# Performance work log

Hardware: AMD Instinct MI355X
Metric: run time of the kernel (lower is better)

## Reference

```python
import jax, jax.numpy as jnp
import numpy as np


def _div_tree_level(n_agents, level):
    # Deterministic reproduction of get_division_tree (seeded shuffle), row `level`.
    rng = np.random.RandomState(0)
    perm = rng.permutation(n_agents)
    max_div = int(np.ceil(np.log2(n_agents)))
    levels = np.zeros((max_div + 1, n_agents), dtype=np.int64)
    for ith in range(1, max_div + 1):
        levels[ith] = levels[ith - 1]
        for j in range(n_agents):
            seg = j // (n_agents / 2 ** ith)
            if int(seg) % 2 == 1:
                levels[ith, j] += 2 ** (ith - 1)
    res = levels[:, perm]  # res_levels[:, i] = levels[:, agent2divitreeindex[i]]
    return res[level]


def setup_inputs() -> dict:
    B, A, D, H, NA = 4096, 32, 512, 512, 32
    LEVEL = 3  # current_level after change_div_tree_level(3): 8 distinct experts
    key = jax.random.key(0)
    ks = jax.random.split(key, 4)
    x0 = jax.random.normal(ks[0], (B, A, D), dtype=jnp.float32)
    W_shared = jax.random.normal(ks[1], (D, H), dtype=jnp.float32) * 0.02
    b_shared = jnp.zeros((H,), jnp.float32)
    W1 = jax.random.normal(ks[2], (A, H, H), dtype=jnp.float32) * 0.02
    b1 = jnp.zeros((A, H), jnp.float32)
    W2 = jax.random.normal(ks[3], (A, H, NA), dtype=jnp.float32) * 0.02
    b2 = jnp.zeros((A, NA), jnp.float32)
    route = jnp.asarray(_div_tree_level(A, LEVEL), dtype=jnp.int32)  # [A] expert id per agent
    return dict(x0=x0, W_shared=W_shared, b_shared=b_shared,
                W1=W1, b1=b1, W2=W2, b2=b2, route=route)


def reference(x0, W_shared, b_shared, W1, b1, W2, b2, route):
    # shared trunk: Linear + ReLU over all agents at once
    x1 = jax.nn.relu(x0 @ W_shared + b_shared)          # [B, A, H]
    # static MoE dispatch: gather each agent's expert weights, batched GEMM per agent slot
    Wg1, bg1 = W1[route], b1[route]                     # [A, H, H], [A, H]
    Wg2, bg2 = W2[route], b2[route]                     # [A, H, NA], [A, NA]
    h = jax.nn.relu(jnp.einsum('bah,ahk->bak', x1, Wg1) + bg1)   # [B, A, H]
    x2 = jnp.einsum('bah,ahk->bak', h, Wg2) + bg2       # [B, A, NA]
    return x2
```

## Files before the change

kernel.cpp:

```cpp
#include <hip/hip_runtime.h>
#include <cstdint>
#include <cstddef>

typedef __bf16 bf16x8 __attribute__((ext_vector_type(8)));
typedef float f32x4 __attribute__((ext_vector_type(4)));
typedef unsigned short u16;
typedef u16 u16x4 __attribute__((ext_vector_type(4)));

__device__ __forceinline__ u16 f2bf(float f) {
  union { float f; unsigned u; } v; v.f = f;
  return (u16)((v.u + 0x7FFFu + ((v.u >> 16) & 1u)) >> 16);
}

__device__ __forceinline__ void gl_lds16(const void* g, void* l) {
  __builtin_amdgcn_global_load_lds((__attribute__((address_space(1))) void*)(g),
                                   (__attribute__((address_space(3))) void*)(l), 16, 0, 0);
}

__global__ void transpose_cvt(const float* __restrict__ in, const int* __restrict__ route,
                              u16* __restrict__ out, int K, int N) {
  __shared__ float t[32][33];
  const int a = blockIdx.z;
  const int src = route ? route[a] : a;
  const float* ip = in + (size_t)src * K * N;
  u16* op = out + (size_t)a * K * N;
  const int k0 = blockIdx.x * 32, n0 = blockIdx.y * 32;
  const int tx = threadIdx.x, ty = threadIdx.y;
#pragma unroll
  for (int i = 0; i < 4; ++i)
    t[ty + i * 8][tx] = ip[(size_t)(k0 + ty + i * 8) * N + n0 + tx];
  __syncthreads();
#pragma unroll
  for (int i = 0; i < 4; ++i)
    op[(size_t)(n0 + ty + i * 8) * K + k0 + tx] = f2bf(t[tx][ty + i * 8]);
}

__global__ __launch_bounds__(512)
void fused_mlp(const float* __restrict__ X0, const u16* __restrict__ Wst,
               const float* __restrict__ bsh, const u16* __restrict__ W1t,
               const float* __restrict__ b1, const u16* __restrict__ W2t,
               const float* __restrict__ b2, const int* __restrict__ route,
               float* __restrict__ Out) {
  __shared__ u16 lds[69632];
  u16* Xs = lds;
  u16* Bp0 = lds + 32768;
  u16* Bp1 = lds + 49152;
  u16* Ap0 = lds + 65536;
  u16* Ap1 = lds + 67584;

  const int tid = threadIdx.x;
  const int w = tid >> 6, l = tid & 63;
  const int r = l & 15, q = l >> 4;
  const int a = blockIdx.y;
  const int b0 = blockIdx.x * 64;
  const int rt = route[a];

  int aoff[4], boff[4];
#pragma unroll
  for (int t = 0; t < 4; ++t) {
    aoff[t] = (t * 16 + r) * 32 + ((q ^ ((r >> 1) & 3)) << 3);
    boff[t] = (w * 64 + t * 16 + r) * 32 + ((q ^ ((r >> 1) & 3)) << 3);
  }

  int bdst[4]; int bsrc[4];
#pragma unroll
  for (int c = 0; c < 4; ++c) {
    const int p2 = c * 512 + tid;
    const int n = p2 >> 2, s = p2 & 3;
    bsrc[c] = n * 512 + ((s ^ ((n >> 1) & 3)) << 3);
    bdst[c] = p2 * 8;
  }

  const int arow = tid >> 3, akq = tid & 7;
  const float* gA = X0 + ((size_t)(b0 + arow) * 32 + a) * 512 + akq * 4;
  const int adst = arow * 32 + (((akq >> 1) ^ ((arow >> 1) & 3)) << 3) + (akq & 1) * 4;

  f32x4 acc[4][4];

#pragma unroll
  for (int mt = 0; mt < 4; ++mt)
#pragma unroll
    for (int nt = 0; nt < 4; ++nt) acc[mt][nt] = (f32x4){0.f, 0.f, 0.f, 0.f};

  float4 av = *(const float4*)gA;
#pragma unroll
  for (int c = 0; c < 4; ++c) gl_lds16(Wst + bsrc[c], &Bp0[bdst[c]]);
  {
    const u16x4 d = { f2bf(av.x), f2bf(av.y), f2bf(av.z), f2bf(av.w) };
    *(u16x4*)&Ap0[adst] = d;
  }
  __syncthreads();

  for (int kt = 0; kt < 16; ++kt) {
    const u16* Bc = (kt & 1) ? Bp1 : Bp0;
    const u16* Ac = (kt & 1) ? Ap1 : Ap0;
    u16* Bn = (kt & 1) ? Bp0 : Bp1;
    u16* An = (kt & 1) ? Ap0 : Ap1;
    if (kt < 15) {
      av = *(const float4*)(gA + (kt + 1) * 32);
#pragma unroll
      for (int c = 0; c < 4; ++c)
        gl_lds16(Wst + bsrc[c] + (kt + 1) * 32, &Bn[bdst[c]]);
    }
    bf16x8 af[4], bv[4];
#pragma unroll
    for (int t = 0; t < 4; ++t) af[t] = *(const bf16x8*)&Ac[aoff[t]];
#pragma unroll
    for (int t = 0; t < 4; ++t) bv[t] = *(const bf16x8*)&Bc[boff[t]];
#pragma unroll
    for (int mt = 0; mt < 4; ++mt)
#pragma unroll
      for (int nt = 0; nt < 4; ++nt)
        acc[mt][nt] = __builtin_amdgcn_mfma_f32_16x16x32_bf16(bv[nt], af[mt], acc[mt][nt], 0, 0, 0);
    if (kt < 15) {
      const u16x4 d = { f2bf(av.x), f2bf(av.y), f2bf(av.z), f2bf(av.w) };
      *(u16x4*)&An[adst] = d;
    }
    __syncthreads();
  }
#pragma unroll
  for (int mt = 0; mt < 4; ++mt) {
    const int m = mt * 16 + r;
#pragma unroll
    for (int nt = 0; nt < 4; ++nt) {
      const int col = w * 64 + nt * 16 + q * 4;
      const int gp = (col >> 3) ^ (m & 7);
      const float4 bb = *(const float4*)&bsh[col];
      const f32x4 v = acc[mt][nt];
      const u16x4 d = { f2bf(fmaxf(v.x + bb.x, 0.f)), f2bf(fmaxf(v.y + bb.y, 0.f)),
                        f2bf(fmaxf(v.z + bb.z, 0.f)), f2bf(fmaxf(v.w + bb.w, 0.f)) };
      *(u16x4*)&Xs[m * 512 + gp * 8 + (q & 1) * 4] = d;
    }
  }

  const u16* W1a = W1t + (size_t)a * 262144;
#pragma unroll
  for (int c = 0; c < 4; ++c) gl_lds16(W1a + bsrc[c], &Bp0[bdst[c]]);
  __syncthreads();

#pragma unroll
  for (int mt = 0; mt < 4; ++mt)
#pragma unroll
    for (int nt = 0; nt < 4; ++nt) acc[mt][nt] = (f32x4){0.f, 0.f, 0.f, 0.f};

  for (int kt = 0; kt < 16; ++kt) {
    const u16* Bc = (kt & 1) ? Bp1 : Bp0;
    u16* Bn = (kt & 1) ? Bp0 : Bp1;
    if (kt < 15) {
#pragma unroll
      for (int c = 0; c < 4; ++c)
        gl_lds16(W1a + bsrc[c] + (kt + 1) * 32, &Bn[bdst[c]]);
    }
    bf16x8 af[4], bv[4];
#pragma unroll
    for (int t = 0; t < 4; ++t) {
      const int m = t * 16 + r;
      af[t] = *(const bf16x8*)&Xs[m * 512 + (((kt * 4 + q) ^ (m & 7)) << 3)];
    }
#pragma unroll
    for (int t = 0; t < 4; ++t) bv[t] = *(const bf16x8*)&Bc[boff[t]];
#pragma unroll
    for (int mt = 0; mt < 4; ++mt)
#pragma unroll
      for (int nt = 0; nt < 4; ++nt)
        acc[mt][nt] = __builtin_amdgcn_mfma_f32_16x16x32_bf16(bv[nt], af[mt], acc[mt][nt], 0, 0, 0);
    __syncthreads();
  }

  const u16* W2a = W2t + (size_t)a * 16384;
#pragma unroll
  for (int c = 0; c < 4; ++c) {
    const int p2 = c * 512 + tid;
    const int n = p2 >> 6, gs = p2 & 63;
    gl_lds16(W2a + (size_t)n * 512 + ((gs ^ (n & 7)) << 3), &Bp0[p2 * 8]);
  }
#pragma unroll
  for (int mt = 0; mt < 4; ++mt) {
    const int m = mt * 16 + r;
#pragma unroll
    for (int nt = 0; nt < 4; ++nt) {
      const int col = w * 64 + nt * 16 + q * 4;
      const int gp = (col >> 3) ^ (m & 7);
      const float4 bb = *(const float4*)&b1[(size_t)rt * 512 + col];
      const f32x4 v = acc[mt][nt];
      const u16x4 d = { f2bf(fmaxf(v.x + bb.x, 0.f)), f2bf(fmaxf(v.y + bb.y, 0.f)),
                        f2bf(fmaxf(v.z + bb.z, 0.f)), f2bf(fmaxf(v.w + bb.w, 0.f)) };
      *(u16x4*)&Xs[m * 512 + gp * 8 + (q & 1) * 4] = d;
    }
  }
  __syncthreads();

  {
    const int mt3 = w & 3, nt3 = w >> 2;
    const int m = mt3 * 16 + r;
    const int n = nt3 * 16 + r;
    f32x4 o = (f32x4){0.f, 0.f, 0.f, 0.f};
#pragma unroll
    for (int kt = 0; kt < 16; ++kt) {
      const bf16x8 af = *(const bf16x8*)&Xs[m * 512 + (((kt * 4 + q) ^ (m & 7)) << 3)];
      const bf16x8 bf = *(const bf16x8*)&Bp0[n * 512 + (((kt * 4 + q) ^ (n & 7)) << 3)];
      o = __builtin_amdgcn_mfma_f32_16x16x32_bf16(bf, af, o, 0, 0, 0);
    }
    const int col = nt3 * 16 + q * 4;
    const float4 bb = *(const float4*)&b2[rt * 32 + col];
    const float4 res = { o.x + bb.x, o.y + bb.y, o.z + bb.z, o.w + bb.w };
    *(float4*)&Out[(size_t)(b0 + m) * 1024 + a * 32 + col] = res;
  }
}

extern "C" void kernel_launch(void* const* d_in, const int* in_sizes, int n_in,
                              void* d_out, int out_size, void* d_ws, size_t ws_size,
                              hipStream_t stream) {
  (void)in_sizes; (void)n_in; (void)out_size; (void)ws_size;
  const float* x0  = (const float*)d_in[0];
  const float* Wsh = (const float*)d_in[1];
  const float* bsh = (const float*)d_in[2];
  const float* W1  = (const float*)d_in[3];
  const float* b1  = (const float*)d_in[4];
  const float* W2  = (const float*)d_in[5];
  const float* b2  = (const float*)d_in[6];
  const int* route = (const int*)d_in[7];
  float* out = (float*)d_out;

  char* ws = (char*)d_ws;
  u16* Wst = (u16*)(ws + 0);
  u16* W1t = (u16*)(ws + 524288);
  u16* W2t = (u16*)(ws + 524288 + 16777216);

  transpose_cvt<<<dim3(16, 16, 1),  dim3(32, 8), 0, stream>>>(Wsh, nullptr, Wst, 512, 512);
  transpose_cvt<<<dim3(16, 16, 32), dim3(32, 8), 0, stream>>>(W1, route, W1t, 512, 512);
  transpose_cvt<<<dim3(16, 1, 32),  dim3(32, 8), 0, stream>>>(W2, route, W2t, 512, 32);
  fused_mlp<<<dim3(64, 32), 512, 0, stream>>>(x0, Wst, bsh, W1t, b1, W2t, b2, route, out);
}
```

Baseline: 618.4 us.

## Pre-swizzle weights into MFMA fragment order and read them directly from global

Weight conversion kernels now write bf16 weights in per-lane MFMA fragment order, so the fused kernel loads B operands straight from global/L2 into registers with register double-buffering instead of staging them through LDS. X0 is loaded and converted into LDS up front in one pass rather than pipelined per k-tile. LDS use drops to a single 64KB activation buffer, and the grid is remapped so blocks sharing an agent land on the same XCD for L2 reuse, with launch bounds raised. This removes many LDS writes and barriers but relies on L2 bandwidth and latency hiding for weight fetches.

```diff
diff --git a/kernel.cpp b/kernel.cpp
--- a/kernel.cpp
+++ b/kernel.cpp
@@ -6,74 +6,105 @@
 typedef float f32x4 __attribute__((ext_vector_type(4)));
 typedef unsigned short u16;
 typedef u16 u16x4 __attribute__((ext_vector_type(4)));
+typedef u16 u16x8 __attribute__((ext_vector_type(8)));
 
 __device__ __forceinline__ u16 f2bf(float f) {
   union { float f; unsigned u; } v; v.f = f;
   return (u16)((v.u + 0x7FFFu + ((v.u >> 16) & 1u)) >> 16);
 }
 
-__device__ __forceinline__ void gl_lds16(const void* g, void* l) {
-  __builtin_amdgcn_global_load_lds((__attribute__((address_space(1))) void*)(g),
-                                   (__attribute__((address_space(3))) void*)(l), 16, 0, 0);
+__global__ void frag_cvt(const float* __restrict__ in, const int* __restrict__ route,
+                         u16* __restrict__ out, int K, int N) {
+  const int a = blockIdx.z;
+  const int src = route ? route[a] : a;
+  const int f = threadIdx.x >> 6, l = threadIdx.x & 63;
+  const int r = l & 15, q = l >> 4;
+  const int kt = blockIdx.x * 4 + f;
+  const int nb = blockIdx.y;
+  const int KT = K >> 5, NB = N >> 4;
+  const float* ip = in + (size_t)src * K * N + (size_t)(kt * 32 + q * 8) * N + nb * 16 + r;
+  u16x8 d;
+#pragma unroll
+  for (int e = 0; e < 8; ++e) d[e] = f2bf(ip[(size_t)e * N]);
+  *(u16x8*)&out[((((size_t)a * NB + nb) * KT + kt) * 64 + l) * 8] = d;
 }
 
-__global__ void transpose_cvt(const float* __restrict__ in, const int* __restrict__ route,
-                              u16* __restrict__ out, int K, int N) {
-  __shared__ float t[32][33];
-  const int a = blockIdx.z;
-  const int src = route ? route[a] : a;
-  const float* ip = in + (size_t)src * K * N;
-  u16* op = out + (size_t)a * K * N;
-  const int k0 = blockIdx.x * 32, n0 = blockIdx.y * 32;
-  const int tx = threadIdx.x, ty = threadIdx.y;
+__device__ __forceinline__ void gemm64(const u16* __restrict__ Bw, const u16* __restrict__ Xs,
+                                       int r, int q, f32x4 acc[4][4]) {
+  bf16x8 bcur[4], bnxt[4];
 #pragma unroll
-  for (int i = 0; i < 4; ++i)
-    t[ty + i * 8][tx] = ip[(size_t)(k0 + ty + i * 8) * N + n0 + tx];
-  __syncthreads();
+  for (int nt = 0; nt < 4; ++nt) bcur[nt] = *(const bf16x8*)(Bw + nt * 8192);
 #pragma unroll
-  for (int i = 0; i < 4; ++i)
-    op[(size_t)(n0 + ty + i * 8) * K + k0 + tx] = f2bf(t[tx][ty + i * 8]);
+  for (int kt = 0; kt < 16; ++kt) {
+    if (kt < 15) {
+#pragma unroll
+      for (int nt = 0; nt < 4; ++nt)
+        bnxt[nt] = *(const bf16x8*)(Bw + nt * 8192 + (kt + 1) * 512);
+    }
+#pragma unroll
+    for (int mt = 0; mt < 4; ++mt) {
+      const int m = mt * 16 + r;
+      const bf16x8 af = *(const bf16x8*)&Xs[m * 512 + ((((kt << 2) + q) ^ (m & 7)) << 3)];
+#pragma unroll
+      for (int nt = 0; nt < 4; ++nt)
+        acc[mt][nt] = __builtin_amdgcn_mfma_f32_16x16x32_bf16(bcur[nt], af, acc[mt][nt], 0, 0, 0);
+    }
+#pragma unroll
+    for (int nt = 0; nt < 4; ++nt) bcur[nt] = bnxt[nt];
+  }
 }
 
-__global__ __launch_bounds__(512)
-void fused_mlp(const float* __restrict__ X0, const u16* __restrict__ Wst,
-               const float* __restrict__ bsh, const u16* __restrict__ W1t,
-               const float* __restrict__ b1, const u16* __restrict__ W2t,
+__device__ __forceinline__ void epi_relu(u16* __restrict__ Xs, const float* __restrict__ bias,
+                                         f32x4 acc[4][4], int w, int r, int q) {
+#pragma unroll
+  for (int mt = 0; mt < 4; ++mt) {
+    const int m = mt * 16 + r;
+#pragma unroll
+    for (int nt = 0; nt < 4; ++nt) {
+      const int col = w * 64 + nt * 16 + q * 4;
+      const int gp = (col >> 3) ^ (m & 7);
+      const float4 bb = *(const float4*)&bias[col];
+      const f32x4 v = acc[mt][nt];
+      const u16x4 d = { f2bf(fmaxf(v.x + bb.x, 0.f)), f2bf(fmaxf(v.y + bb.y, 0.f)),
+                        f2bf(fmaxf(v.z + bb.z, 0.f)), f2bf(fmaxf(v.w + bb.w, 0.f)) };
+      *(u16x4*)&Xs[m * 512 + gp * 8 + (q & 1) * 4] = d;
+    }
+  }
+}
+
+__global__ __launch_bounds__(512, 4)
+void fused_mlp(const float* __restrict__ X0, const u16* __restrict__ Wsf,
+               const float* __restrict__ bsh, const u16* __restrict__ W1f,
+               const float* __restrict__ b1, const u16* __restrict__ W2f,
                const float* __restrict__ b2, const int* __restrict__ route,
                float* __restrict__ Out) {
-  __shared__ u16 lds[69632];
-  u16* Xs = lds;
-  u16* Bp0 = lds + 32768;
-  u16* Bp1 = lds + 49152;
-  u16* Ap0 = lds + 65536;
-  u16* Ap1 = lds + 67584;
+  __shared__ u16 Xs[64 * 512];
 
   const int tid = threadIdx.x;
   const int w = tid >> 6, l = tid & 63;
   const int r = l & 15, q = l >> 4;
-  const int a = blockIdx.y;
-  const int b0 = blockIdx.x * 64;
+
+  const int bid = blockIdx.x;
+  const int xcd = bid & 7, idx = bid >> 3;
+  const int a = (xcd << 2) | (idx >> 6);
+  const int b0 = (idx & 63) << 6;
   const int rt = route[a];
 
-  int aoff[4], boff[4];
+  {
+    const float* gx = X0 + ((size_t)b0 * 32 + a) * 512;
 #pragma unroll
-  for (int t = 0; t < 4; ++t) {
-    aoff[t] = (t * 16 + r) * 32 + ((q ^ ((r >> 1) & 3)) << 3);
-    boff[t] = (w * 64 + t * 16 + r) * 32 + ((q ^ ((r >> 1) & 3)) << 3);
+    for (int i = 0; i < 8; ++i) {
+      const int lin = i * 512 + tid;
+      const int m = lin >> 6, g = lin & 63;
+      const float* p = gx + (size_t)m * (32 * 512) + g * 8;
+      const float4 u = *(const float4*)p;
+      const float4 v = *(const float4*)(p + 4);
+      const u16x8 d = { f2bf(u.x), f2bf(u.y), f2bf(u.z), f2bf(u.w),
+                        f2bf(v.x), f2bf(v.y), f2bf(v.z), f2bf(v.w) };
+      *(u16x8*)&Xs[m * 512 + ((g ^ (m & 7)) << 3)] = d;
+    }
   }
-
-  int bdst[4]; int bsrc[4];
-#pragma unroll
-  for (int c = 0; c < 4; ++c) {
-    const int p2 = c * 512 + tid;
-    const int n = p2 >> 2, s = p2 & 3;
-    bsrc[c] = n * 512 + ((s ^ ((n >> 1) & 3)) << 3);
-    bdst[c] = p2 * 8;
-  }
-
-  const int arow = tid >> 3, akq = tid & 7;
-  const float* gA = X0 + ((size_t)(b0 + arow) * 32 + a) * 512 + akq * 4;
-  const int adst = arow * 32 + (((akq >> 1) ^ ((arow >> 1) & 3)) << 3) + (akq & 1) * 4;
+  __syncthreads();
 
   f32x4 acc[4][4];
 
@@ -81,127 +112,32 @@
   for (int mt = 0; mt < 4; ++mt)
 #pragma unroll
     for (int nt = 0; nt < 4; ++nt) acc[mt][nt] = (f32x4){0.f, 0.f, 0.f, 0.f};
-
-  float4 av = *(const float4*)gA;
-#pragma unroll
-  for (int c = 0; c < 4; ++c) gl_lds16(Wst + bsrc[c], &Bp0[bdst[c]]);
-  {
-    const u16x4 d = { f2bf(av.x), f2bf(av.y), f2bf(av.z), f2bf(av.w) };
-    *(u16x4*)&Ap0[adst] = d;
-  }
+  gemm64(Wsf + (w << 15) + l * 8, Xs, r, q, acc);
   __syncthreads();
-
-  for (int kt = 0; kt < 16; ++kt) {
-    const u16* Bc = (kt & 1) ? Bp1 : Bp0;
-    const u16* Ac = (kt & 1) ? Ap1 : Ap0;
-    u16* Bn = (kt & 1) ? Bp0 : Bp1;
-    u16* An = (kt & 1) ? Ap0 : Ap1;
-    if (kt < 15) {
-      av = *(const float4*)(gA + (kt + 1) * 32);
-#pragma unroll
-      for (int c = 0; c < 4; ++c)
-        gl_lds16(Wst + bsrc[c] + (kt + 1) * 32, &Bn[bdst[c]]);
-    }
-    bf16x8 af[4], bv[4];
-#pragma unroll
-    for (int t = 0; t < 4; ++t) af[t] = *(const bf16x8*)&Ac[aoff[t]];
-#pragma unroll
-    for (int t = 0; t < 4; ++t) bv[t] = *(const bf16x8*)&Bc[boff[t]];
-#pragma unroll
-    for (int mt = 0; mt < 4; ++mt)
-#pragma unroll
-      for (int nt = 0; nt < 4; ++nt)
-        acc[mt][nt] = __builtin_amdgcn_mfma_f32_16x16x32_bf16(bv[nt], af[mt], acc[mt][nt], 0, 0, 0);
-    if (kt < 15) {
-      const u16x4 d = { f2bf(av.x), f2bf(av.y), f2bf(av.z), f2bf(av.w) };
-      *(u16x4*)&An[adst] = d;
-    }
-    __syncthreads();
-  }
-#pragma unroll
-  for (int mt = 0; mt < 4; ++mt) {
-    const int m = mt * 16 + r;
-#pragma unroll
-    for (int nt = 0; nt < 4; ++nt) {
-      const int col = w * 64 + nt * 16 + q * 4;
-      const int gp = (col >> 3) ^ (m & 7);
-      const float4 bb = *(const float4*)&bsh[col];
-      const f32x4 v = acc[mt][nt];
-      const u16x4 d = { f2bf(fmaxf(v.x + bb.x, 0.f)), f2bf(fmaxf(v.y + bb.y, 0.f)),
-                        f2bf(fmaxf(v.z + bb.z, 0.f)), f2bf(fmaxf(v.w + bb.w, 0.f)) };
-      *(u16x4*)&Xs[m * 512 + gp * 8 + (q & 1) * 4] = d;
-    }
-  }
-
-  const u16* W1a = W1t + (size_t)a * 262144;
-#pragma unroll
-  for (int c = 0; c < 4; ++c) gl_lds16(W1a + bsrc[c], &Bp0[bdst[c]]);
+  epi_relu(Xs, bsh, acc, w, r, q);
   __syncthreads();
 
 #pragma unroll
   for (int mt = 0; mt < 4; ++mt)
 #pragma unroll
     for (int nt = 0; nt < 4; ++nt) acc[mt][nt] = (f32x4){0.f, 0.f, 0.f, 0.f};
-
-  for (int kt = 0; kt < 16; ++kt) {
-    const u16* Bc = (kt & 1) ? Bp1 : Bp0;
-    u16* Bn = (kt & 1) ? Bp0 : Bp1;
-    if (kt < 15) {
-#pragma unroll
-      for (int c = 0; c < 4; ++c)
-        gl_lds16(W1a + bsrc[c] + (kt + 1) * 32, &Bn[bdst[c]]);
-    }
-    bf16x8 af[4], bv[4];
-#pragma unroll
-    for (int t = 0; t < 4; ++t) {
-      const int m = t * 16 + r;
-      af[t] = *(const bf16x8*)&Xs[m * 512 + (((kt * 4 + q) ^ (m & 7)) << 3)];
-    }
-#pragma unroll
-    for (int t = 0; t < 4; ++t) bv[t] = *(const bf16x8*)&Bc[boff[t]];
-#pragma unroll
-    for (int mt = 0; mt < 4; ++mt)
-#pragma unroll
-      for (int nt = 0; nt < 4; ++nt)
-        acc[mt][nt] = __builtin_amdgcn_mfma_f32_16x16x32_bf16(bv[nt], af[mt], acc[mt][nt], 0, 0, 0);
-    __syncthreads();
-  }
-
-  const u16* W2a = W2t + (size_t)a * 16384;
-#pragma unroll
-  for (int c = 0; c < 4; ++c) {
-    const int p2 = c * 512 + tid;
-    const int n = p2 >> 6, gs = p2 & 63;
-    gl_lds16(W2a + (size_t)n * 512 + ((gs ^ (n & 7)) << 3), &Bp0[p2 * 8]);
-  }
-#pragma unroll
-  for (int mt = 0; mt < 4; ++mt) {
-    const int m = mt * 16 + r;
-#pragma unroll
-    for (int nt = 0; nt < 4; ++nt) {
-      const int col = w * 64 + nt * 16 + q * 4;
-      const int gp = (col >> 3) ^ (m & 7);
-      const float4 bb = *(const float4*)&b1[(size_t)rt * 512 + col];
-      const f32x4 v = acc[mt][nt];
-      const u16x4 d = { f2bf(fmaxf(v.x + bb.x, 0.f)), f2bf(fmaxf(v.y + bb.y, 0.f)),
-                        f2bf(fmaxf(v.z + bb.z, 0.f)), f2bf(fmaxf(v.w + bb.w, 0.f)) };
-      *(u16x4*)&Xs[m * 512 + gp * 8 + (q & 1) * 4] = d;
-    }
-  }
+  gemm64(W1f + (size_t)a * 262144 + (w << 15) + l * 8, Xs, r, q, acc);
+  __syncthreads();
+  epi_relu(Xs, b1 + (size_t)rt * 512, acc, w, r, q);
   __syncthreads();
 
   {
     const int mt3 = w & 3, nt3 = w >> 2;
     const int m = mt3 * 16 + r;
-    const int n = nt3 * 16 + r;
+    const u16* B2 = W2f + (size_t)a * 16384 + (nt3 << 13) + l * 8;
     f32x4 o = (f32x4){0.f, 0.f, 0.f, 0.f};
 #pragma unroll
     for (int kt = 0; kt < 16; ++kt) {
-      const bf16x8 af = *(const bf16x8*)&Xs[m * 512 + (((kt * 4 + q) ^ (m & 7)) << 3)];
-      const bf16x8 bf = *(const bf16x8*)&Bp0[n * 512 + (((kt * 4 + q) ^ (n & 7)) << 3)];
+      const bf16x8 af = *(const bf16x8*)&Xs[m * 512 + ((((kt << 2) + q) ^ (m & 7)) << 3)];
+      const bf16x8 bf = *(const bf16x8*)(B2 + (kt << 9));
       o = __builtin_amdgcn_mfma_f32_16x16x32_bf16(bf, af, o, 0, 0, 0);
     }
-    const int col = nt3 * 16 + q * 4;
+    const int col = (nt3 << 4) + (q << 2);
     const float4 bb = *(const float4*)&b2[rt * 32 + col];
     const float4 res = { o.x + bb.x, o.y + bb.y, o.z + bb.z, o.w + bb.w };
     *(float4*)&Out[(size_t)(b0 + m) * 1024 + a * 32 + col] = res;
@@ -223,12 +159,12 @@
   float* out = (float*)d_out;
 
   char* ws = (char*)d_ws;
-  u16* Wst = (u16*)(ws + 0);
-  u16* W1t = (u16*)(ws + 524288);
-  u16* W2t = (u16*)(ws + 524288 + 16777216);
+  u16* Wsf = (u16*)(ws + 0);
+  u16* W1f = (u16*)(ws + 524288);
+  u16* W2f = (u16*)(ws + 524288 + 16777216);
 
-  transpose_cvt<<<dim3(16, 16, 1),  dim3(32, 8), 0, stream>>>(Wsh, nullptr, Wst, 512, 512);
-  transpose_cvt<<<dim3(16, 16, 32), dim3(32, 8), 0, stream>>>(W1, route, W1t, 512, 512);
-  transpose_cvt<<<dim3(16, 1, 32),  dim3(32, 8), 0, stream>>>(W2, route, W2t, 512, 32);
-  fused_mlp<<<dim3(64, 32), 512, 0, stream>>>(x0, Wst, bsh, W1t, b1, W2t, b2, route, out);
+  frag_cvt<<<dim3(4, 32, 1),  256, 0, stream>>>(Wsh, nullptr, Wsf, 512, 512);
+  frag_cvt<<<dim3(4, 32, 32), 256, 0, stream>>>(W1, route, W1f, 512, 512);
+  frag_cvt<<<dim3(4, 2, 32),  256, 0, stream>>>(W2, route, W2f, 512, 32);
+  fused_mlp<<<dim3(2048), 512, 0, stream>>>(x0, Wsf, bsh, W1f, b1, W2f, b2, route, out);
 }
```

After: 555.0 us. 1.11x faster.
